# Performance work log

Hardware: AMD Instinct MI355X
Metric: run time of the kernel (lower is better)

## Reference

```python
import jax, jax.numpy as jnp
import numpy as np


def setup_inputs() -> dict:
    key = jax.random.key(0)
    ks = jax.random.split(key, 4)
    B, H, W, C = 4, 64, 64, 256
    Ck = C // 8
    x = jax.random.normal(ks[0], (B, H, W, C), dtype=jnp.float32)
    Wf = jax.random.normal(ks[1], (C, Ck), dtype=jnp.float32) * (1.0 / np.sqrt(C))
    Wg = jax.random.normal(ks[2], (C, Ck), dtype=jnp.float32) * (1.0 / np.sqrt(C))
    Wh = jax.random.normal(ks[3], (C, C), dtype=jnp.float32) * (1.0 / np.sqrt(C))
    bf = jnp.zeros((Ck,), jnp.float32)
    bg = jnp.zeros((Ck,), jnp.float32)
    bh = jnp.zeros((C,), jnp.float32)
    gamma = jnp.ones((1,), jnp.float32)
    return {"x": x, "Wf": Wf, "bf": bf, "Wg": Wg, "bg": bg, "Wh": Wh, "bh": bh, "gamma": gamma}


def reference(x, Wf, bf, Wg, bg, Wh, bh, gamma):
    B, H, W, C = x.shape
    N = H * W
    xf = x.reshape(B, N, C)  # hw_flatten; 1x1 conv == per-pixel matmul
    f = xf @ Wf + bf          # [B, N, C//8] (keys)
    g = xf @ Wg + bg          # [B, N, C//8] (queries)
    h = xf @ Wh + bh          # [B, N, C]    (values)
    s = jnp.einsum('bnk,bmk->bnm', g, f)   # [B, N, N], no scaling (as in source)
    b = jax.nn.softmax(s, axis=-1)
    o = jnp.einsum('bnm,bmc->bnc', b, h)   # [B, N, C]
    y = gamma * o.reshape(B, H, W, C) + x
    return y
```

## Files before the change

kernel.cpp:

```cpp
#include <hip/hip_runtime.h>
#include <stdint.h>

typedef short short8 __attribute__((ext_vector_type(8)));
typedef short short4_t __attribute__((ext_vector_type(4)));
typedef float f32x4 __attribute__((ext_vector_type(4)));

__device__ __forceinline__ float bf2f(unsigned short u) {
    union { unsigned int i; float f; } v; v.i = ((unsigned int)u) << 16; return v.f;
}
__device__ __forceinline__ unsigned short f2bf(float f) {
    union { float f; unsigned int i; } v; v.f = f;
    return (unsigned short)((v.i + 0x8000u) >> 16);
}

__global__ __launch_bounds__(256) void k_pre(const float* __restrict__ x,
                                             const float* __restrict__ Wf,
                                             const float* __restrict__ Wg,
                                             const float* __restrict__ Wh,
                                             unsigned short* __restrict__ xh,
                                             unsigned short* __restrict__ xl,
                                             unsigned short* __restrict__ wTh,
                                             unsigned short* __restrict__ wTl) {
    if (blockIdx.x < 2048) {
        int gid = blockIdx.x * 256 + threadIdx.x;
        const float* src = x + (size_t)gid * 8;
        f32x4 a0 = *(const f32x4*)src;
        f32x4 a1 = *(const f32x4*)(src + 4);
        short8 sh, sl;
#pragma unroll
        for (int j = 0; j < 4; ++j) {
            unsigned short h0 = f2bf(a0[j]);
            sh[j] = (short)h0; sl[j] = (short)f2bf(a0[j] - bf2f(h0));
            unsigned short h1 = f2bf(a1[j]);
            sh[4 + j] = (short)h1; sl[4 + j] = (short)f2bf(a1[j] - bf2f(h1));
        }
        *(short8*)&xh[(size_t)gid * 8] = sh;
        *(short8*)&xl[(size_t)gid * 8] = sl;
    } else {
        int col = blockIdx.x - 2048;
        int k = threadIdx.x;
        float v;
        if (col < 32) v = Wf[k * 32 + col];
        else if (col < 64) v = Wg[k * 32 + (col - 32)];
        else v = Wh[k * 256 + (col - 64)];
        unsigned short h = f2bf(v);
        wTh[col * 256 + k] = h;
        if (col < 64) wTl[col * 256 + k] = f2bf(v - bf2f(h));
    }
}

__global__ __launch_bounds__(256) void k_proj(
    const unsigned short* __restrict__ xh,
    const unsigned short* __restrict__ xl,
    const unsigned short* __restrict__ wTh,
    const unsigned short* __restrict__ wTl,
    const float* __restrict__ bfb,
    const float* __restrict__ bgb,
    const float* __restrict__ bhb,
    unsigned short* __restrict__ fKh,
    unsigned short* __restrict__ fKl,
    unsigned short* __restrict__ gQh,
    unsigned short* __restrict__ gQl,
    unsigned short* __restrict__ hT) {
    __shared__ short sm[4 * 64 * 72];
    int tid = threadIdx.x;
    int wave = tid >> 6, lane = tid & 63, lq = lane & 15, quad = lane >> 4;
    int rt = blockIdx.x;
    const unsigned short* xhb = xh + (size_t)rt * 64 * 256;
    const unsigned short* xlb = xl + (size_t)rt * 64 * 256;
    f32x4 zero4 = {0.f, 0.f, 0.f, 0.f};

    if (blockIdx.y < 4) {
        const int XO = 0, WO = 64 * 136;
        int cb = blockIdx.y;
        const unsigned short* wbase = wTh + (size_t)(64 + cb * 64) * 256;
        f32x4 acc[4] = {zero4, zero4, zero4, zero4};

        for (int ph = 0; ph < 2; ++ph) {
            int k0 = ph * 128;
            __syncthreads();
#pragma unroll
            for (int u = 0; u < 4; ++u) {
                int q = u * 256 + tid;
                int row = q >> 4, kc = q & 15;
                *(short8*)&sm[XO + row * 136 + kc * 8] =
                    *(const short8*)&xhb[row * 256 + k0 + kc * 8];
                *(short8*)&sm[WO + row * 136 + kc * 8] =
                    *(const short8*)&wbase[row * 256 + k0 + kc * 8];
            }
            __syncthreads();
#pragma unroll
            for (int ks = 0; ks < 4; ++ks) {
                short8 a = *(const short8*)&sm[XO + (wave * 16 + lq) * 136 + ks * 32 + quad * 8];
#pragma unroll
                for (int ct = 0; ct < 4; ++ct) {
                    short8 bfr = *(const short8*)&sm[WO + (lq + 16 * ct) * 136 + ks * 32 + quad * 8];
                    acc[ct] = __builtin_amdgcn_mfma_f32_16x16x32_bf16(a, bfr, acc[ct], 0, 0, 0);
                }
            }
        }

        int rowl = wave * 16 + quad * 4;
        int grow0 = rt * 64;
        int bidx = grow0 >> 12, n0 = (grow0 & 4095) + rowl;
#pragma unroll
        for (int ct = 0; ct < 4; ++ct) {
            int c = cb * 64 + lq + 16 * ct;
            float bias = bhb[c];
            short4_t pk;
#pragma unroll
            for (int r = 0; r < 4; ++r) pk[r] = (short)f2bf(acc[ct][r] + bias);
            size_t a8 = (((size_t)(bidx * 16 + (c >> 4)) * 128 + (n0 >> 5)) * 64 +
                         ((n0 & 31) >> 3) * 16 + (c & 15)) * 8 + (n0 & 7);
            *(short4_t*)&hT[a8] = pk;
        }
    } else {
        const int XH = 0, XL = 64 * 72, WH = 2 * 64 * 72, WL = 3 * 64 * 72;
        f32x4 acc[4] = {zero4, zero4, zero4, zero4};

        for (int ph = 0; ph < 4; ++ph) {
            int k0 = ph * 64;
            __syncthreads();
#pragma unroll
            for (int u = 0; u < 2; ++u) {
                int q = u * 256 + tid;
                int row = q >> 3, kc = q & 7;
                *(short8*)&sm[XH + row * 72 + kc * 8] =
                    *(const short8*)&xhb[row * 256 + k0 + kc * 8];
                *(short8*)&sm[XL + row * 72 + kc * 8] =
                    *(const short8*)&xlb[row * 256 + k0 + kc * 8];
                *(short8*)&sm[WH + row * 72 + kc * 8] =
                    *(const short8*)&wTh[row * 256 + k0 + kc * 8];
                *(short8*)&sm[WL + row * 72 + kc * 8] =
                    *(const short8*)&wTl[row * 256 + k0 + kc * 8];
            }
            __syncthreads();
#pragma unroll
            for (int ks = 0; ks < 2; ++ks) {
                short8 ah = *(const short8*)&sm[XH + (wave * 16 + lq) * 72 + ks * 32 + quad * 8];
                short8 al = *(const short8*)&sm[XL + (wave * 16 + lq) * 72 + ks * 32 + quad * 8];
#pragma unroll
                for (int ct = 0; ct < 4; ++ct) {
                    short8 bh = *(const short8*)&sm[WH + (lq + 16 * ct) * 72 + ks * 32 + quad * 8];
                    short8 bl = *(const short8*)&sm[WL + (lq + 16 * ct) * 72 + ks * 32 + quad * 8];
                    acc[ct] = __builtin_amdgcn_mfma_f32_16x16x32_bf16(ah, bh, acc[ct], 0, 0, 0);
                    acc[ct] = __builtin_amdgcn_mfma_f32_16x16x32_bf16(al, bh, acc[ct], 0, 0, 0);
                    acc[ct] = __builtin_amdgcn_mfma_f32_16x16x32_bf16(ah, bl, acc[ct], 0, 0, 0);
                }
            }
        }

        int rowl = wave * 16 + quad * 4;
#pragma unroll
        for (int ct = 0; ct < 4; ++ct) {
            int coll = lq + 16 * ct;
#pragma unroll
            for (int r = 0; r < 4; ++r) {
                int grow = rt * 64 + rowl + r;
                int bidx = grow >> 12, n = grow & 4095;
                float v = acc[ct][r];
                size_t o = (size_t)(bidx * 256 + (n >> 4)) * 512 +
                           (((coll & 31) >> 3) * 16 + (n & 15)) * 8 + (coll & 7);
                if (coll < 32) {
                    v += bfb[coll];
                    unsigned short h = f2bf(v);
                    fKh[o] = h;
                    fKl[o] = f2bf(v - bf2f(h));
                } else {
                    int cg = coll - 32;
                    size_t og = (size_t)(bidx * 256 + (n >> 4)) * 512 +
                                ((cg >> 3) * 16 + (n & 15)) * 8 + (cg & 7);
                    v += bgb[cg];
                    unsigned short h = f2bf(v);
                    gQh[og] = h;
                    gQl[og] = f2bf(v - bf2f(h));
                }
            }
        }
    }
}

#define PSTR 72
__global__ __launch_bounds__(512, 4) void k_attn(
    const unsigned short* __restrict__ fKh,
    const unsigned short* __restrict__ fKl,
    const unsigned short* __restrict__ gQh,
    const unsigned short* __restrict__ gQl,
    const unsigned short* __restrict__ hT,
    const float* __restrict__ x,
    const float* __restrict__ gam_p,
    float* __restrict__ out) {
    __shared__ short Ps[2][32 * PSTR];
    __shared__ short Fb[2][2][2048];
    __shared__ float Lred[2][16][4];
    int tid = threadIdx.x;
    int wave = tid >> 6, lane = tid & 63, lq = lane & 15, quad = lane >> 4;
    int b = blockIdx.x & 3;
    int qt = blockIdx.x >> 2;
    int rs = wave >> 2;
    int kt4 = wave & 3;

    const unsigned short* fhB = fKh + (size_t)b * 131072;
    const unsigned short* flB = fKl + (size_t)b * 131072;
    const unsigned short* hB  = hT + (size_t)b * 1048576;
    int lchunk = quad * 16 + lq;

    f32x4 zero4 = {0.f, 0.f, 0.f, 0.f};
    f32x4 acc[4];
#pragma unroll
    for (int i = 0; i < 4; ++i) acc[i] = zero4;
    float l_part[4] = {0.f, 0.f, 0.f, 0.f};

    int gtile = b * 256 + qt * 2 + rs;
    short8 ghfrag = *(const short8*)&gQh[(size_t)gtile * 512 + lchunk * 8];
    short8 glfrag = *(const short8*)&gQl[(size_t)gtile * 512 + lchunk * 8];

    int sid = tid & 255;
    int hl = tid >> 8;
    const unsigned short* fB0 = hl ? flB : fhB;

    *(short8*)&Fb[0][hl][sid * 8] = *(const short8*)&fB0[(size_t)sid * 8];
    __syncthreads();

    for (int kt = 0; kt < 64; ++kt) {
        int p = kt & 1;
        int nkt = kt < 63 ? kt + 1 : kt;
        short8 fn = *(const short8*)&fB0[(size_t)nkt * 2048 + sid * 8];

        int k0 = kt * 2;
        short8 hb[2][2];
#pragma unroll
        for (int ct = 0; ct < 2; ++ct) {
            int ctile = wave * 2 + ct;
#pragma unroll
            for (int kk = 0; kk < 2; ++kk)
                hb[ct][kk] = *(const short8*)
                    &hB[(((size_t)ctile * 128 + k0 + kk) * 64 + lchunk) * 8];
        }

        short8 fh = *(const short8*)&Fb[p][0][kt4 * 512 + lchunk * 8];
        short8 fl = *(const short8*)&Fb[p][1][kt4 * 512 + lchunk * 8];
        __builtin_amdgcn_s_setprio(1);
        f32x4 S = __builtin_amdgcn_mfma_f32_16x16x32_bf16(ghfrag, fh, zero4, 0, 0, 0);
        S = __builtin_amdgcn_mfma_f32_16x16x32_bf16(glfrag, fh, S, 0, 0, 0);
        S = __builtin_amdgcn_mfma_f32_16x16x32_bf16(ghfrag, fl, S, 0, 0, 0);
        __builtin_amdgcn_s_setprio(0);

#pragma unroll
        for (int r = 0; r < 4; ++r) {
            S[r] = __expf(S[r]);
            l_part[r] += S[r];
        }

#pragma unroll
        for (int r = 0; r < 4; ++r)
            Ps[p][(rs * 16 + quad * 4 + r) * PSTR + kt4 * 16 + lq] =
                (short)f2bf(S[r]);

        *(short8*)&Fb[1 - p][hl][sid * 8] = fn;

        __syncthreads();

        __builtin_amdgcn_s_setprio(1);
#pragma unroll
        for (int rb = 0; rb < 2; ++rb) {
            short8 pa0 = *(const short8*)&Ps[p][(rb * 16 + lq) * PSTR + quad * 8];
            short8 pa1 = *(const short8*)&Ps[p][(rb * 16 + lq) * PSTR + 32 + quad * 8];
#pragma unroll
            for (int ct = 0; ct < 2; ++ct) {
                acc[rb * 2 + ct] = __builtin_amdgcn_mfma_f32_16x16x32_bf16(pa0, hb[ct][0], acc[rb * 2 + ct], 0, 0, 0);
                acc[rb * 2 + ct] = __builtin_amdgcn_mfma_f32_16x16x32_bf16(pa1, hb[ct][1], acc[rb * 2 + ct], 0, 0, 0);
            }
        }
        __builtin_amdgcn_s_setprio(0);
    }

#pragma unroll
    for (int r = 0; r < 4; ++r) {
        float s = l_part[r];
        s += __shfl_xor(s, 1);
        s += __shfl_xor(s, 2);
        s += __shfl_xor(s, 4);
        s += __shfl_xor(s, 8);
        if (lq == 0) Lred[rs][quad * 4 + r][kt4] = s;
    }
    __syncthreads();

    float gam = gam_p[0];
#pragma unroll
    for (int rb = 0; rb < 2; ++rb)
#pragma unroll
        for (int r = 0; r < 4; ++r) {
            float l = Lred[rb][quad * 4 + r][0] + Lred[rb][quad * 4 + r][1] +
                      Lred[rb][quad * 4 + r][2] + Lred[rb][quad * 4 + r][3];
            float linv = 1.0f / l;
            int n = qt * 32 + rb * 16 + quad * 4 + r;
            size_t rowo = ((size_t)(b * 4096 + n)) * 256;
#pragma unroll
            for (int ct = 0; ct < 2; ++ct) {
                int c = wave * 32 + ct * 16 + lq;
                out[rowo + c] = gam * (acc[rb * 2 + ct][r] * linv) + x[rowo + c];
            }
        }
}

extern "C" void kernel_launch(void* const* d_in, const int* in_sizes, int n_in,
                              void* d_out, int out_size, void* d_ws, size_t ws_size,
                              hipStream_t stream) {
    const float* x   = (const float*)d_in[0];
    const float* Wf  = (const float*)d_in[1];
    const float* bfb = (const float*)d_in[2];
    const float* Wg  = (const float*)d_in[3];
    const float* bgb = (const float*)d_in[4];
    const float* Wh  = (const float*)d_in[5];
    const float* bhb = (const float*)d_in[6];
    const float* gam = (const float*)d_in[7];
    float* out = (float*)d_out;

    char* ws = (char*)d_ws;
    const size_t MI = 1u << 20;
    unsigned short* xh  = (unsigned short*)(ws);
    unsigned short* xl  = (unsigned short*)(ws + 8 * MI);
    unsigned short* fKh = (unsigned short*)(ws + 16 * MI);
    unsigned short* fKl = (unsigned short*)(ws + 17 * MI);
    unsigned short* gQh = (unsigned short*)(ws + 18 * MI);
    unsigned short* gQl = (unsigned short*)(ws + 19 * MI);
    unsigned short* hT  = (unsigned short*)(ws + 20 * MI);
    unsigned short* wTh = (unsigned short*)(ws + 28 * MI);
    unsigned short* wTl = (unsigned short*)(ws + 28 * MI + 160 * 1024);

    k_pre<<<dim3(2368), dim3(256), 0, stream>>>(x, Wf, Wg, Wh, xh, xl, wTh, wTl);
    k_proj<<<dim3(256, 5), dim3(256), 0, stream>>>(xh, xl, wTh, wTl, bfb, bgb, bhb,
                                                   fKh, fKl, gQh, gQl, hT);
    k_attn<<<dim3(512), dim3(512), 0, stream>>>(fKh, fKl, gQh, gQl, hT,
                                                x, gam, out);
}
```

Measured before the change: 152.0 us.

## Double key tile per iteration and register-prefetch K/V, dropping LDS staging of keys

```diff
diff --git a/kernel.cpp b/kernel.cpp
--- a/kernel.cpp
+++ b/kernel.cpp
@@ -180,7 +180,7 @@
     }
 }
 
-#define PSTR 72
+#define PSTR 136
 __global__ __launch_bounds__(512, 4) void k_attn(
     const unsigned short* __restrict__ fKh,
     const unsigned short* __restrict__ fKl,
@@ -191,7 +191,6 @@
     const float* __restrict__ gam_p,
     float* __restrict__ out) {
     __shared__ short Ps[2][32 * PSTR];
-    __shared__ short Fb[2][2][2048];
     __shared__ float Lred[2][16][4];
     int tid = threadIdx.x;
     int wave = tid >> 6, lane = tid & 63, lq = lane & 15, quad = lane >> 4;
@@ -199,11 +198,11 @@
     int qt = blockIdx.x >> 2;
     int rs = wave >> 2;
     int kt4 = wave & 3;
+    int lchunk = quad * 16 + lq;
 
     const unsigned short* fhB = fKh + (size_t)b * 131072;
     const unsigned short* flB = fKl + (size_t)b * 131072;
     const unsigned short* hB  = hT + (size_t)b * 1048576;
-    int lchunk = quad * 16 + lq;
 
     f32x4 zero4 = {0.f, 0.f, 0.f, 0.f};
     f32x4 acc[4];
@@ -215,64 +214,78 @@
     short8 ghfrag = *(const short8*)&gQh[(size_t)gtile * 512 + lchunk * 8];
     short8 glfrag = *(const short8*)&gQl[(size_t)gtile * 512 + lchunk * 8];
 
-    int sid = tid & 255;
-    int hl = tid >> 8;
-    const unsigned short* fB0 = hl ? flB : fhB;
-
-    *(short8*)&Fb[0][hl][sid * 8] = *(const short8*)&fB0[(size_t)sid * 8];
-    __syncthreads();
-
-    for (int kt = 0; kt < 64; ++kt) {
-        int p = kt & 1;
-        int nkt = kt < 63 ? kt + 1 : kt;
-        short8 fn = *(const short8*)&fB0[(size_t)nkt * 2048 + sid * 8];
-
-        int k0 = kt * 2;
-        short8 hb[2][2];
-#pragma unroll
-        for (int ct = 0; ct < 2; ++ct) {
-            int ctile = wave * 2 + ct;
-#pragma unroll
-            for (int kk = 0; kk < 2; ++kk)
-                hb[ct][kk] = *(const short8*)
-                    &hB[(((size_t)ctile * 128 + k0 + kk) * 64 + lchunk) * 8];
-        }
-
-        short8 fh = *(const short8*)&Fb[p][0][kt4 * 512 + lchunk * 8];
-        short8 fl = *(const short8*)&Fb[p][1][kt4 * 512 + lchunk * 8];
+    size_t fo0 = (size_t)kt4 * 512 + lchunk * 8;
+    const unsigned short* hp = hB + (size_t)(wave * 2) * 65536;
+    size_t ho0 = (size_t)lchunk * 8;
+
+    short8 fh0 = *(const short8*)&fhB[fo0];
+    short8 fh1 = *(const short8*)&fhB[fo0 + 2048];
+    short8 fl0 = *(const short8*)&flB[fo0];
+    short8 fl1 = *(const short8*)&flB[fo0 + 2048];
+    short8 hb[2][4];
+#pragma unroll
+    for (int ct = 0; ct < 2; ++ct)
+#pragma unroll
+        for (int kk = 0; kk < 4; ++kk)
+            hb[ct][kk] = *(const short8*)&hp[ho0 + ct * 65536 + kk * 512];
+
+    for (int t = 0; t < 32; ++t) {
+        int p = t & 1;
         __builtin_amdgcn_s_setprio(1);
-        f32x4 S = __builtin_amdgcn_mfma_f32_16x16x32_bf16(ghfrag, fh, zero4, 0, 0, 0);
-        S = __builtin_amdgcn_mfma_f32_16x16x32_bf16(glfrag, fh, S, 0, 0, 0);
-        S = __builtin_amdgcn_mfma_f32_16x16x32_bf16(ghfrag, fl, S, 0, 0, 0);
+        f32x4 S0 = __builtin_amdgcn_mfma_f32_16x16x32_bf16(ghfrag, fh0, zero4, 0, 0, 0);
+        f32x4 S1 = __builtin_amdgcn_mfma_f32_16x16x32_bf16(ghfrag, fh1, zero4, 0, 0, 0);
+        S0 = __builtin_amdgcn_mfma_f32_16x16x32_bf16(glfrag, fh0, S0, 0, 0, 0);
+        S1 = __builtin_amdgcn_mfma_f32_16x16x32_bf16(glfrag, fh1, S1, 0, 0, 0);
+        S0 = __builtin_amdgcn_mfma_f32_16x16x32_bf16(ghfrag, fl0, S0, 0, 0, 0);
+        S1 = __builtin_amdgcn_mfma_f32_16x16x32_bf16(ghfrag, fl1, S1, 0, 0, 0);
         __builtin_amdgcn_s_setprio(0);
 
+        {
+            size_t fo = (size_t)(t < 31 ? t + 1 : t) * 4096 + fo0;
+            fh0 = *(const short8*)&fhB[fo];
+            fh1 = *(const short8*)&fhB[fo + 2048];
+            fl0 = *(const short8*)&flB[fo];
+            fl1 = *(const short8*)&flB[fo + 2048];
+        }
+
 #pragma unroll
         for (int r = 0; r < 4; ++r) {
-            S[r] = __expf(S[r]);
-            l_part[r] += S[r];
-        }
-
-#pragma unroll
-        for (int r = 0; r < 4; ++r)
-            Ps[p][(rs * 16 + quad * 4 + r) * PSTR + kt4 * 16 + lq] =
-                (short)f2bf(S[r]);
-
-        *(short8*)&Fb[1 - p][hl][sid * 8] = fn;
+            S0[r] = __expf(S0[r]);
+            S1[r] = __expf(S1[r]);
+            l_part[r] += S0[r] + S1[r];
+        }
+#pragma unroll
+        for (int r = 0; r < 4; ++r) {
+            int row = rs * 16 + quad * 4 + r;
+            Ps[p][row * PSTR + kt4 * 16 + lq] = (short)f2bf(S0[r]);
+            Ps[p][row * PSTR + 64 + kt4 * 16 + lq] = (short)f2bf(S1[r]);
+        }
 
         __syncthreads();
 
         __builtin_amdgcn_s_setprio(1);
 #pragma unroll
         for (int rb = 0; rb < 2; ++rb) {
-            short8 pa0 = *(const short8*)&Ps[p][(rb * 16 + lq) * PSTR + quad * 8];
-            short8 pa1 = *(const short8*)&Ps[p][(rb * 16 + lq) * PSTR + 32 + quad * 8];
-#pragma unroll
-            for (int ct = 0; ct < 2; ++ct) {
-                acc[rb * 2 + ct] = __builtin_amdgcn_mfma_f32_16x16x32_bf16(pa0, hb[ct][0], acc[rb * 2 + ct], 0, 0, 0);
-                acc[rb * 2 + ct] = __builtin_amdgcn_mfma_f32_16x16x32_bf16(pa1, hb[ct][1], acc[rb * 2 + ct], 0, 0, 0);
+            short8 pa[4];
+#pragma unroll
+            for (int kk = 0; kk < 4; ++kk)
+                pa[kk] = *(const short8*)&Ps[p][(rb * 16 + lq) * PSTR + kk * 32 + quad * 8];
+#pragma unroll
+            for (int kk = 0; kk < 4; ++kk) {
+                acc[rb * 2 + 0] = __builtin_amdgcn_mfma_f32_16x16x32_bf16(pa[kk], hb[0][kk], acc[rb * 2 + 0], 0, 0, 0);
+                acc[rb * 2 + 1] = __builtin_amdgcn_mfma_f32_16x16x32_bf16(pa[kk], hb[1][kk], acc[rb * 2 + 1], 0, 0, 0);
             }
         }
         __builtin_amdgcn_s_setprio(0);
+
+        {
+            size_t ho = (size_t)(t < 31 ? t + 1 : t) * 2048 + ho0;
+#pragma unroll
+            for (int ct = 0; ct < 2; ++ct)
+#pragma unroll
+                for (int kk = 0; kk < 4; ++kk)
+                    hb[ct][kk] = *(const short8*)&hp[ho + ct * 65536 + kk * 512];
+        }
     }
 
 #pragma unroll
```

Result: slower. 158.2 us (+4.0%).

## Software-pipeline attention loop so PV MFMAs overlap next QK^T tile

Applied to the files above, without the earlier changes.

```diff
diff --git a/kernel.cpp b/kernel.cpp
--- a/kernel.cpp
+++ b/kernel.cpp
@@ -199,11 +199,11 @@
     int qt = blockIdx.x >> 2;
     int rs = wave >> 2;
     int kt4 = wave & 3;
+    int lchunk = quad * 16 + lq;
 
     const unsigned short* fhB = fKh + (size_t)b * 131072;
     const unsigned short* flB = fKl + (size_t)b * 131072;
     const unsigned short* hB  = hT + (size_t)b * 1048576;
-    int lchunk = quad * 16 + lq;
 
     f32x4 zero4 = {0.f, 0.f, 0.f, 0.f};
     f32x4 acc[4];
@@ -222,21 +222,39 @@
     *(short8*)&Fb[0][hl][sid * 8] = *(const short8*)&fB0[(size_t)sid * 8];
     __syncthreads();
 
-    for (int kt = 0; kt < 64; ++kt) {
-        int p = kt & 1;
-        int nkt = kt < 63 ? kt + 1 : kt;
-        short8 fn = *(const short8*)&fB0[(size_t)nkt * 2048 + sid * 8];
-
-        int k0 = kt * 2;
-        short8 hb[2][2];
-#pragma unroll
-        for (int ct = 0; ct < 2; ++ct) {
-            int ctile = wave * 2 + ct;
-#pragma unroll
-            for (int kk = 0; kk < 2; ++kk)
-                hb[ct][kk] = *(const short8*)
-                    &hB[(((size_t)ctile * 128 + k0 + kk) * 64 + lchunk) * 8];
-        }
+    short8 hc00, hc01, hc10, hc11;
+    hc00 = *(const short8*)&hB[(((size_t)(wave * 2 + 0) * 128 + 0) * 64 + lchunk) * 8];
+    hc01 = *(const short8*)&hB[(((size_t)(wave * 2 + 0) * 128 + 1) * 64 + lchunk) * 8];
+    hc10 = *(const short8*)&hB[(((size_t)(wave * 2 + 1) * 128 + 0) * 64 + lchunk) * 8];
+    hc11 = *(const short8*)&hB[(((size_t)(wave * 2 + 1) * 128 + 1) * 64 + lchunk) * 8];
+
+    {
+        short8 fh = *(const short8*)&Fb[0][0][kt4 * 512 + lchunk * 8];
+        short8 fl = *(const short8*)&Fb[0][1][kt4 * 512 + lchunk * 8];
+        f32x4 S = __builtin_amdgcn_mfma_f32_16x16x32_bf16(ghfrag, fh, zero4, 0, 0, 0);
+        S = __builtin_amdgcn_mfma_f32_16x16x32_bf16(glfrag, fh, S, 0, 0, 0);
+        S = __builtin_amdgcn_mfma_f32_16x16x32_bf16(ghfrag, fl, S, 0, 0, 0);
+#pragma unroll
+        for (int r = 0; r < 4; ++r) {
+            S[r] = __expf(S[r]);
+            l_part[r] += S[r];
+            Ps[0][(rs * 16 + quad * 4 + r) * PSTR + kt4 * 16 + lq] = (short)f2bf(S[r]);
+        }
+        short8 fn = *(const short8*)&fB0[(size_t)2048 + sid * 8];
+        *(short8*)&Fb[1][hl][sid * 8] = fn;
+    }
+    __syncthreads();
+
+    for (int i = 1; i < 64; ++i) {
+        int p = i & 1;
+
+        int k0 = i * 2;
+        short8 hn00 = *(const short8*)&hB[(((size_t)(wave * 2 + 0) * 128 + k0 + 0) * 64 + lchunk) * 8];
+        short8 hn01 = *(const short8*)&hB[(((size_t)(wave * 2 + 0) * 128 + k0 + 1) * 64 + lchunk) * 8];
+        short8 hn10 = *(const short8*)&hB[(((size_t)(wave * 2 + 1) * 128 + k0 + 0) * 64 + lchunk) * 8];
+        short8 hn11 = *(const short8*)&hB[(((size_t)(wave * 2 + 1) * 128 + k0 + 1) * 64 + lchunk) * 8];
+        int nf = (i < 63) ? i + 1 : i;
+        short8 fn = *(const short8*)&fB0[(size_t)nf * 2048 + sid * 8];
 
         short8 fh = *(const short8*)&Fb[p][0][kt4 * 512 + lchunk * 8];
         short8 fl = *(const short8*)&Fb[p][1][kt4 * 512 + lchunk * 8];
@@ -244,36 +262,43 @@
         f32x4 S = __builtin_amdgcn_mfma_f32_16x16x32_bf16(ghfrag, fh, zero4, 0, 0, 0);
         S = __builtin_amdgcn_mfma_f32_16x16x32_bf16(glfrag, fh, S, 0, 0, 0);
         S = __builtin_amdgcn_mfma_f32_16x16x32_bf16(ghfrag, fl, S, 0, 0, 0);
+
+#pragma unroll
+        for (int rb = 0; rb < 2; ++rb) {
+            short8 pa0 = *(const short8*)&Ps[1 - p][(rb * 16 + lq) * PSTR + quad * 8];
+            short8 pa1 = *(const short8*)&Ps[1 - p][(rb * 16 + lq) * PSTR + 32 + quad * 8];
+            acc[rb * 2 + 0] = __builtin_amdgcn_mfma_f32_16x16x32_bf16(pa0, hc00, acc[rb * 2 + 0], 0, 0, 0);
+            acc[rb * 2 + 0] = __builtin_amdgcn_mfma_f32_16x16x32_bf16(pa1, hc01, acc[rb * 2 + 0], 0, 0, 0);
+            acc[rb * 2 + 1] = __builtin_amdgcn_mfma_f32_16x16x32_bf16(pa0, hc10, acc[rb * 2 + 1], 0, 0, 0);
+            acc[rb * 2 + 1] = __builtin_amdgcn_mfma_f32_16x16x32_bf16(pa1, hc11, acc[rb * 2 + 1], 0, 0, 0);
+        }
         __builtin_amdgcn_s_setprio(0);
 
 #pragma unroll
         for (int r = 0; r < 4; ++r) {
             S[r] = __expf(S[r]);
             l_part[r] += S[r];
-        }
-
-#pragma unroll
-        for (int r = 0; r < 4; ++r)
-            Ps[p][(rs * 16 + quad * 4 + r) * PSTR + kt4 * 16 + lq] =
-                (short)f2bf(S[r]);
+            Ps[p][(rs * 16 + quad * 4 + r) * PSTR + kt4 * 16 + lq] = (short)f2bf(S[r]);
+        }
 
         *(short8*)&Fb[1 - p][hl][sid * 8] = fn;
 
+        hc00 = hn00; hc01 = hn01; hc10 = hn10; hc11 = hn11;
+
         __syncthreads();
-
-        __builtin_amdgcn_s_setprio(1);
-#pragma unroll
-        for (int rb = 0; rb < 2; ++rb) {
-            short8 pa0 = *(const short8*)&Ps[p][(rb * 16 + lq) * PSTR + quad * 8];
-            short8 pa1 = *(const short8*)&Ps[p][(rb * 16 + lq) * PSTR + 32 + quad * 8];
-#pragma unroll
-            for (int ct = 0; ct < 2; ++ct) {
-                acc[rb * 2 + ct] = __builtin_amdgcn_mfma_f32_16x16x32_bf16(pa0, hb[ct][0], acc[rb * 2 + ct], 0, 0, 0);
-                acc[rb * 2 + ct] = __builtin_amdgcn_mfma_f32_16x16x32_bf16(pa1, hb[ct][1], acc[rb * 2 + ct], 0, 0, 0);
-            }
-        }
-        __builtin_amdgcn_s_setprio(0);
-    }
+    }
+
+    __builtin_amdgcn_s_setprio(1);
+#pragma unroll
+    for (int rb = 0; rb < 2; ++rb) {
+        short8 pa0 = *(const short8*)&Ps[1][(rb * 16 + lq) * PSTR + quad * 8];
+        short8 pa1 = *(const short8*)&Ps[1][(rb * 16 + lq) * PSTR + 32 + quad * 8];
+        acc[rb * 2 + 0] = __builtin_amdgcn_mfma_f32_16x16x32_bf16(pa0, hc00, acc[rb * 2 + 0], 0, 0, 0);
+        acc[rb * 2 + 0] = __builtin_amdgcn_mfma_f32_16x16x32_bf16(pa1, hc01, acc[rb * 2 + 0], 0, 0, 0);
+        acc[rb * 2 + 1] = __builtin_amdgcn_mfma_f32_16x16x32_bf16(pa0, hc10, acc[rb * 2 + 1], 0, 0, 0);
+        acc[rb * 2 + 1] = __builtin_amdgcn_mfma_f32_16x16x32_bf16(pa1, hc11, acc[rb * 2 + 1], 0, 0, 0);
+    }
+    __builtin_amdgcn_s_setprio(0);
 
 #pragma unroll
     for (int r = 0; r < 4; ++r) {
```

Result: slower. 158.7 us (+4.4%).

## Fuse x bf16 split into projection and split attention keys across blocks

Applied to the files above, without the earlier changes.

```diff
diff --git a/kernel.cpp b/kernel.cpp
--- a/kernel.cpp
+++ b/kernel.cpp
@@ -13,45 +13,24 @@
     return (unsigned short)((v.i + 0x8000u) >> 16);
 }
 
-__global__ __launch_bounds__(256) void k_pre(const float* __restrict__ x,
-                                             const float* __restrict__ Wf,
-                                             const float* __restrict__ Wg,
-                                             const float* __restrict__ Wh,
-                                             unsigned short* __restrict__ xh,
-                                             unsigned short* __restrict__ xl,
-                                             unsigned short* __restrict__ wTh,
-                                             unsigned short* __restrict__ wTl) {
-    if (blockIdx.x < 2048) {
-        int gid = blockIdx.x * 256 + threadIdx.x;
-        const float* src = x + (size_t)gid * 8;
-        f32x4 a0 = *(const f32x4*)src;
-        f32x4 a1 = *(const f32x4*)(src + 4);
-        short8 sh, sl;
-#pragma unroll
-        for (int j = 0; j < 4; ++j) {
-            unsigned short h0 = f2bf(a0[j]);
-            sh[j] = (short)h0; sl[j] = (short)f2bf(a0[j] - bf2f(h0));
-            unsigned short h1 = f2bf(a1[j]);
-            sh[4 + j] = (short)h1; sl[4 + j] = (short)f2bf(a1[j] - bf2f(h1));
-        }
-        *(short8*)&xh[(size_t)gid * 8] = sh;
-        *(short8*)&xl[(size_t)gid * 8] = sl;
-    } else {
-        int col = blockIdx.x - 2048;
-        int k = threadIdx.x;
-        float v;
-        if (col < 32) v = Wf[k * 32 + col];
-        else if (col < 64) v = Wg[k * 32 + (col - 32)];
-        else v = Wh[k * 256 + (col - 64)];
-        unsigned short h = f2bf(v);
-        wTh[col * 256 + k] = h;
-        if (col < 64) wTl[col * 256 + k] = f2bf(v - bf2f(h));
-    }
+__global__ __launch_bounds__(256) void k_prew(const float* __restrict__ Wf,
+                                              const float* __restrict__ Wg,
+                                              const float* __restrict__ Wh,
+                                              unsigned short* __restrict__ wTh,
+                                              unsigned short* __restrict__ wTl) {
+    int col = blockIdx.x;
+    int k = threadIdx.x;
+    float v;
+    if (col < 32) v = Wf[k * 32 + col];
+    else if (col < 64) v = Wg[k * 32 + (col - 32)];
+    else v = Wh[k * 256 + (col - 64)];
+    unsigned short h = f2bf(v);
+    wTh[col * 256 + k] = h;
+    if (col < 64) wTl[col * 256 + k] = f2bf(v - bf2f(h));
 }
 
 __global__ __launch_bounds__(256) void k_proj(
-    const unsigned short* __restrict__ xh,
-    const unsigned short* __restrict__ xl,
+    const float* __restrict__ x,
     const unsigned short* __restrict__ wTh,
     const unsigned short* __restrict__ wTl,
     const float* __restrict__ bfb,
@@ -66,8 +45,7 @@
     int tid = threadIdx.x;
     int wave = tid >> 6, lane = tid & 63, lq = lane & 15, quad = lane >> 4;
     int rt = blockIdx.x;
-    const unsigned short* xhb = xh + (size_t)rt * 64 * 256;
-    const unsigned short* xlb = xl + (size_t)rt * 64 * 256;
+    const float* xb = x + (size_t)rt * 64 * 256;
     f32x4 zero4 = {0.f, 0.f, 0.f, 0.f};
 
     if (blockIdx.y < 4) {
@@ -83,8 +61,16 @@
             for (int u = 0; u < 4; ++u) {
                 int q = u * 256 + tid;
                 int row = q >> 4, kc = q & 15;
-                *(short8*)&sm[XO + row * 136 + kc * 8] =
-                    *(const short8*)&xhb[row * 256 + k0 + kc * 8];
+                const float* xs = &xb[row * 256 + k0 + kc * 8];
+                f32x4 a0 = *(const f32x4*)xs;
+                f32x4 a1 = *(const f32x4*)(xs + 4);
+                short8 sh;
+#pragma unroll
+                for (int j = 0; j < 4; ++j) {
+                    sh[j] = (short)f2bf(a0[j]);
+                    sh[4 + j] = (short)f2bf(a1[j]);
+                }
+                *(short8*)&sm[XO + row * 136 + kc * 8] = sh;
                 *(short8*)&sm[WO + row * 136 + kc * 8] =
                     *(const short8*)&wbase[row * 256 + k0 + kc * 8];
             }
@@ -125,10 +111,19 @@
             for (int u = 0; u < 2; ++u) {
                 int q = u * 256 + tid;
                 int row = q >> 3, kc = q & 7;
-                *(short8*)&sm[XH + row * 72 + kc * 8] =
-                    *(const short8*)&xhb[row * 256 + k0 + kc * 8];
-                *(short8*)&sm[XL + row * 72 + kc * 8] =
-                    *(const short8*)&xlb[row * 256 + k0 + kc * 8];
+                const float* xs = &xb[row * 256 + k0 + kc * 8];
+                f32x4 a0 = *(const f32x4*)xs;
+                f32x4 a1 = *(const f32x4*)(xs + 4);
+                short8 sh, sl;
+#pragma unroll
+                for (int j = 0; j < 4; ++j) {
+                    unsigned short h0 = f2bf(a0[j]);
+                    sh[j] = (short)h0; sl[j] = (short)f2bf(a0[j] - bf2f(h0));
+                    unsigned short h1 = f2bf(a1[j]);
+                    sh[4 + j] = (short)h1; sl[4 + j] = (short)f2bf(a1[j] - bf2f(h1));
+                }
+                *(short8*)&sm[XH + row * 72 + kc * 8] = sh;
+                *(short8*)&sm[XL + row * 72 + kc * 8] = sl;
                 *(short8*)&sm[WH + row * 72 + kc * 8] =
                     *(const short8*)&wTh[row * 256 + k0 + kc * 8];
                 *(short8*)&sm[WL + row * 72 + kc * 8] =
@@ -187,92 +182,95 @@
     const unsigned short* __restrict__ gQh,
     const unsigned short* __restrict__ gQl,
     const unsigned short* __restrict__ hT,
-    const float* __restrict__ x,
-    const float* __restrict__ gam_p,
-    float* __restrict__ out) {
-    __shared__ short Ps[2][32 * PSTR];
+    float* __restrict__ pacc0,
+    float* __restrict__ pacc1,
+    float* __restrict__ pl) {
+    __shared__ short Ps[2][64 * PSTR];
     __shared__ short Fb[2][2][2048];
-    __shared__ float Lred[2][16][4];
+    __shared__ float Lred[4][16][2];
     int tid = threadIdx.x;
     int wave = tid >> 6, lane = tid & 63, lq = lane & 15, quad = lane >> 4;
     int b = blockIdx.x & 3;
-    int qt = blockIdx.x >> 2;
-    int rs = wave >> 2;
-    int kt4 = wave & 3;
+    int rest = blockIdx.x >> 2;
+    int qt = rest & 63;
+    int ks = rest >> 6;
+    int rs = wave >> 1;
+    int kh = wave & 1;
+    int lchunk = quad * 16 + lq;
 
     const unsigned short* fhB = fKh + (size_t)b * 131072;
     const unsigned short* flB = fKl + (size_t)b * 131072;
     const unsigned short* hB  = hT + (size_t)b * 1048576;
-    int lchunk = quad * 16 + lq;
+    float* pacc = ks ? pacc1 : pacc0;
+    float* plb  = pl + ks * 16384;
 
     f32x4 zero4 = {0.f, 0.f, 0.f, 0.f};
-    f32x4 acc[4];
-#pragma unroll
-    for (int i = 0; i < 4; ++i) acc[i] = zero4;
+    f32x4 acc[8];
+#pragma unroll
+    for (int i = 0; i < 8; ++i) acc[i] = zero4;
     float l_part[4] = {0.f, 0.f, 0.f, 0.f};
 
-    int gtile = b * 256 + qt * 2 + rs;
+    int gtile = b * 256 + qt * 4 + rs;
     short8 ghfrag = *(const short8*)&gQh[(size_t)gtile * 512 + lchunk * 8];
     short8 glfrag = *(const short8*)&gQl[(size_t)gtile * 512 + lchunk * 8];
 
     int sid = tid & 255;
     int hl = tid >> 8;
     const unsigned short* fB0 = hl ? flB : fhB;
-
-    *(short8*)&Fb[0][hl][sid * 8] = *(const short8*)&fB0[(size_t)sid * 8];
+    int ft0 = ks * 128;
+
+    *(short8*)&Fb[0][hl][sid * 8] = *(const short8*)&fB0[(size_t)ft0 * 512 + sid * 8];
     __syncthreads();
 
-    for (int kt = 0; kt < 64; ++kt) {
+    for (int kt = 0; kt < 32; ++kt) {
         int p = kt & 1;
-        int nkt = kt < 63 ? kt + 1 : kt;
-        short8 fn = *(const short8*)&fB0[(size_t)nkt * 2048 + sid * 8];
-
-        int k0 = kt * 2;
-        short8 hb[2][2];
-#pragma unroll
-        for (int ct = 0; ct < 2; ++ct) {
-            int ctile = wave * 2 + ct;
-#pragma unroll
-            for (int kk = 0; kk < 2; ++kk)
-                hb[ct][kk] = *(const short8*)
-                    &hB[(((size_t)ctile * 128 + k0 + kk) * 64 + lchunk) * 8];
-        }
-
-        short8 fh = *(const short8*)&Fb[p][0][kt4 * 512 + lchunk * 8];
-        short8 fl = *(const short8*)&Fb[p][1][kt4 * 512 + lchunk * 8];
-        __builtin_amdgcn_s_setprio(1);
-        f32x4 S = __builtin_amdgcn_mfma_f32_16x16x32_bf16(ghfrag, fh, zero4, 0, 0, 0);
-        S = __builtin_amdgcn_mfma_f32_16x16x32_bf16(glfrag, fh, S, 0, 0, 0);
-        S = __builtin_amdgcn_mfma_f32_16x16x32_bf16(ghfrag, fl, S, 0, 0, 0);
-        __builtin_amdgcn_s_setprio(0);
+        int nft = ft0 + (kt < 31 ? kt + 1 : kt) * 4;
+        short8 fn = *(const short8*)&fB0[(size_t)nft * 512 + sid * 8];
+
+        int k0 = ks * 64 + kt * 2;
+        int ct0 = wave * 2;
+        short8 hb00 = *(const short8*)&hB[(((size_t)(ct0 + 0) * 128 + k0 + 0) * 64 + lchunk) * 8];
+        short8 hb01 = *(const short8*)&hB[(((size_t)(ct0 + 0) * 128 + k0 + 1) * 64 + lchunk) * 8];
+        short8 hb10 = *(const short8*)&hB[(((size_t)(ct0 + 1) * 128 + k0 + 0) * 64 + lchunk) * 8];
+        short8 hb11 = *(const short8*)&hB[(((size_t)(ct0 + 1) * 128 + k0 + 1) * 64 + lchunk) * 8];
+
+        short8 fh0 = *(const short8*)&Fb[p][0][(kh * 2 + 0) * 512 + lchunk * 8];
+        short8 fl0 = *(const short8*)&Fb[p][1][(kh * 2 + 0) * 512 + lchunk * 8];
+        short8 fh1 = *(const short8*)&Fb[p][0][(kh * 2 + 1) * 512 + lchunk * 8];
+        short8 fl1 = *(const short8*)&Fb[p][1][(kh * 2 + 1) * 512 + lchunk * 8];
+        f32x4 S0 = __builtin_amdgcn_mfma_f32_16x16x32_bf16(ghfrag, fh0, zero4, 0, 0, 0);
+        f32x4 S1 = __builtin_amdgcn_mfma_f32_16x16x32_bf16(ghfrag, fh1, zero4, 0, 0, 0);
+        S0 = __builtin_amdgcn_mfma_f32_16x16x32_bf16(glfrag, fh0, S0, 0, 0, 0);
+        S1 = __builtin_amdgcn_mfma_f32_16x16x32_bf16(glfrag, fh1, S1, 0, 0, 0);
+        S0 = __builtin_amdgcn_mfma_f32_16x16x32_bf16(ghfrag, fl0, S0, 0, 0, 0);
+        S1 = __builtin_amdgcn_mfma_f32_16x16x32_bf16(ghfrag, fl1, S1, 0, 0, 0);
 
 #pragma unroll
         for (int r = 0; r < 4; ++r) {
-            S[r] = __expf(S[r]);
-            l_part[r] += S[r];
-        }
-
-#pragma unroll
-        for (int r = 0; r < 4; ++r)
-            Ps[p][(rs * 16 + quad * 4 + r) * PSTR + kt4 * 16 + lq] =
-                (short)f2bf(S[r]);
+            S0[r] = __expf(S0[r]);
+            S1[r] = __expf(S1[r]);
+            l_part[r] += S0[r] + S1[r];
+        }
+#pragma unroll
+        for (int r = 0; r < 4; ++r) {
+            int row = rs * 16 + quad * 4 + r;
+            Ps[p][row * PSTR + (kh * 2 + 0) * 16 + lq] = (short)f2bf(S0[r]);
+            Ps[p][row * PSTR + (kh * 2 + 1) * 16 + lq] = (short)f2bf(S1[r]);
+        }
 
         *(short8*)&Fb[1 - p][hl][sid * 8] = fn;
 
         __syncthreads();
 
-        __builtin_amdgcn_s_setprio(1);
-#pragma unroll
-        for (int rb = 0; rb < 2; ++rb) {
+#pragma unroll
+        for (int rb = 0; rb < 4; ++rb) {
             short8 pa0 = *(const short8*)&Ps[p][(rb * 16 + lq) * PSTR + quad * 8];
             short8 pa1 = *(const short8*)&Ps[p][(rb * 16 + lq) * PSTR + 32 + quad * 8];
-#pragma unroll
-            for (int ct = 0; ct < 2; ++ct) {
-                acc[rb * 2 + ct] = __builtin_amdgcn_mfma_f32_16x16x32_bf16(pa0, hb[ct][0], acc[rb * 2 + ct], 0, 0, 0);
-                acc[rb * 2 + ct] = __builtin_amdgcn_mfma_f32_16x16x32_bf16(pa1, hb[ct][1], acc[rb * 2 + ct], 0, 0, 0);
-            }
-        }
-        __builtin_amdgcn_s_setprio(0);
+            acc[rb * 2 + 0] = __builtin_amdgcn_mfma_f32_16x16x32_bf16(pa0, hb00, acc[rb * 2 + 0], 0, 0, 0);
+            acc[rb * 2 + 0] = __builtin_amdgcn_mfma_f32_16x16x32_bf16(pa1, hb01, acc[rb * 2 + 0], 0, 0, 0);
+            acc[rb * 2 + 1] = __builtin_amdgcn_mfma_f32_16x16x32_bf16(pa0, hb10, acc[rb * 2 + 1], 0, 0, 0);
+            acc[rb * 2 + 1] = __builtin_amdgcn_mfma_f32_16x16x32_bf16(pa1, hb11, acc[rb * 2 + 1], 0, 0, 0);
+        }
     }
 
 #pragma unroll
@@ -282,26 +280,47 @@
         s += __shfl_xor(s, 2);
         s += __shfl_xor(s, 4);
         s += __shfl_xor(s, 8);
-        if (lq == 0) Lred[rs][quad * 4 + r][kt4] = s;
+        if (lq == 0) Lred[rs][quad * 4 + r][kh] = s;
     }
     __syncthreads();
-
+    if (kh == 0 && lq == 0) {
+#pragma unroll
+        for (int r = 0; r < 4; ++r) {
+            int rl = quad * 4 + r;
+            plb[b * 4096 + qt * 64 + rs * 16 + rl] = Lred[rs][rl][0] + Lred[rs][rl][1];
+        }
+    }
+
+#pragma unroll
+    for (int rb = 0; rb < 4; ++rb)
+#pragma unroll
+        for (int ct = 0; ct < 2; ++ct) {
+            int c = wave * 32 + ct * 16 + lq;
+#pragma unroll
+            for (int r = 0; r < 4; ++r) {
+                int n = qt * 64 + rb * 16 + quad * 4 + r;
+                pacc[((size_t)(b * 4096 + n)) * 256 + c] = acc[rb * 2 + ct][r];
+            }
+        }
+}
+
+__global__ __launch_bounds__(256) void k_combine(
+    const float* __restrict__ x,
+    const float* __restrict__ gam_p,
+    const float* __restrict__ pacc1,
+    const float* __restrict__ pl,
+    float* __restrict__ out) {
+    int gid = blockIdx.x * 256 + threadIdx.x;
+    int row = gid >> 6;
+    f32x4 a0 = *(const f32x4*)&out[(size_t)gid * 4];
+    f32x4 a1 = *(const f32x4*)&pacc1[(size_t)gid * 4];
+    f32x4 xv = *(const f32x4*)&x[(size_t)gid * 4];
+    float linv = 1.0f / (pl[row] + pl[16384 + row]);
     float gam = gam_p[0];
-#pragma unroll
-    for (int rb = 0; rb < 2; ++rb)
-#pragma unroll
-        for (int r = 0; r < 4; ++r) {
-            float l = Lred[rb][quad * 4 + r][0] + Lred[rb][quad * 4 + r][1] +
-                      Lred[rb][quad * 4 + r][2] + Lred[rb][quad * 4 + r][3];
-            float linv = 1.0f / l;
-            int n = qt * 32 + rb * 16 + quad * 4 + r;
-            size_t rowo = ((size_t)(b * 4096 + n)) * 256;
-#pragma unroll
-            for (int ct = 0; ct < 2; ++ct) {
-                int c = wave * 32 + ct * 16 + lq;
-                out[rowo + c] = gam * (acc[rb * 2 + ct][r] * linv) + x[rowo + c];
-            }
-        }
+    f32x4 o;
+#pragma unroll
+    for (int j = 0; j < 4; ++j) o[j] = gam * ((a0[j] + a1[j]) * linv) + xv[j];
+    *(f32x4*)&out[(size_t)gid * 4] = o;
 }
 
 extern "C" void kernel_launch(void* const* d_in, const int* in_sizes, int n_in,
@@ -319,19 +338,20 @@
 
     char* ws = (char*)d_ws;
     const size_t MI = 1u << 20;
-    unsigned short* xh  = (unsigned short*)(ws);
-    unsigned short* xl  = (unsigned short*)(ws + 8 * MI);
-    unsigned short* fKh = (unsigned short*)(ws + 16 * MI);
-    unsigned short* fKl = (unsigned short*)(ws + 17 * MI);
-    unsigned short* gQh = (unsigned short*)(ws + 18 * MI);
-    unsigned short* gQl = (unsigned short*)(ws + 19 * MI);
-    unsigned short* hT  = (unsigned short*)(ws + 20 * MI);
-    unsigned short* wTh = (unsigned short*)(ws + 28 * MI);
-    unsigned short* wTl = (unsigned short*)(ws + 28 * MI + 160 * 1024);
-
-    k_pre<<<dim3(2368), dim3(256), 0, stream>>>(x, Wf, Wg, Wh, xh, xl, wTh, wTl);
-    k_proj<<<dim3(256, 5), dim3(256), 0, stream>>>(xh, xl, wTh, wTl, bfb, bgb, bhb,
+    unsigned short* fKh = (unsigned short*)(ws);
+    unsigned short* fKl = (unsigned short*)(ws + 1 * MI);
+    unsigned short* gQh = (unsigned short*)(ws + 2 * MI);
+    unsigned short* gQl = (unsigned short*)(ws + 3 * MI);
+    unsigned short* hT  = (unsigned short*)(ws + 4 * MI);
+    unsigned short* wTh = (unsigned short*)(ws + 12 * MI);
+    unsigned short* wTl = (unsigned short*)(ws + 12 * MI + 160 * 1024);
+    float* pacc1 = (float*)(ws + 13 * MI);
+    float* pl    = (float*)(ws + 29 * MI);
+
+    k_prew<<<dim3(320), dim3(256), 0, stream>>>(Wf, Wg, Wh, wTh, wTl);
+    k_proj<<<dim3(256, 5), dim3(256), 0, stream>>>(x, wTh, wTl, bfb, bgb, bhb,
                                                    fKh, fKl, gQh, gQl, hT);
     k_attn<<<dim3(512), dim3(512), 0, stream>>>(fKh, fKl, gQh, gQl, hT,
-                                                x, gam, out);
-}
+                                                out, pacc1, pl);
+    k_combine<<<dim3(4096), dim3(256), 0, stream>>>(x, gam, pacc1, pl, out);
+}
```

Result: no change. 154.1 us (+1.4%).
